# Kernel optimization log

Hardware: AMD Instinct MI355X
Metric: run time of the kernel (lower is better)

## Reference

```python
import jax, jax.numpy as jnp
import numpy as np

NUM_CLASSES = 19
EPS_MEAN = 1e-6   # torch: denominator eps in per-class mean
EPS_COS = 1e-8    # torch CosineSimilarity default eps


def _nearest_resize_labels(target, H, W):
    # torch nn.Upsample(mode='nearest'): in_idx = floor(out_idx * in / out)
    th, tw = target.shape[1], target.shape[2]
    ih = (jnp.arange(H) * th) // H
    iw = (jnp.arange(W) * tw) // W
    return target[:, ih][:, :, iw]  # [B,H,W]


def _class_centers(feat, lab):
    # feat: [B,C,H,W]; lab: [B,H,W] int. Single-pass segment mean by class,
    # then scatter means back to pixels whose label is in [0, NUM_CLASSES).
    B, C, H, W = feat.shape
    f = feat.reshape(B, C, H * W)                 # [B,C,N]
    l = lab.reshape(B, H * W)                      # [B,N]
    onehot = jax.nn.one_hot(l, NUM_CLASSES, dtype=feat.dtype)  # [B,N,K]; out-of-range -> all-zero row
    sums = jnp.einsum('bcn,bnk->bck', f, onehot)   # per-class channel sums
    counts = onehot.sum(axis=1)                    # [B,K]
    means = sums / (counts[:, None, :] + EPS_MEAN) # [B,C,K]
    gathered = jnp.einsum('bck,bnk->bcn', means, onehot)  # mean at each valid pixel, 0 elsewhere
    valid = (l >= 0) & (l < NUM_CLASSES)           # [B,N]
    center = jnp.where(valid[:, None, :], gathered, f)
    return center.reshape(B, C, H, W)


def _cosine_dim1(a, b):
    # torch CosineSimilarity(dim=1): dot / (max(||a||,eps) * max(||b||,eps))
    num = (a * b).sum(axis=1)
    na = jnp.sqrt((a * a).sum(axis=1))
    nb = jnp.sqrt((b * b).sum(axis=1))
    return num / (jnp.maximum(na, EPS_COS) * jnp.maximum(nb, EPS_COS))


def setup_inputs() -> dict:
    key = jax.random.key(0)
    k1, k2, k3 = jax.random.split(key, 3)
    B, C, H, W = 8, 512, 64, 64
    preds_S = jax.random.normal(k1, (B, C, H, W), dtype=jnp.float32)
    preds_T = jax.random.normal(k2, (B, C, H, W), dtype=jnp.float32)
    target = jax.random.randint(k3, (B, 512, 512), 0, NUM_CLASSES, dtype=jnp.int64)
    return {"preds_S": preds_S, "preds_T": preds_T, "target": target}


def reference(preds_S, preds_T, target):
    H, W = preds_S.shape[2], preds_S.shape[3]
    lab = _nearest_resize_labels(target, H, W)     # [B,H,W]
    center_S = _class_centers(preds_S, lab)
    center_T = _class_centers(preds_T, lab)
    pcsim_S = _cosine_dim1(preds_S, center_S)      # [B,H,W]
    pcsim_T = _cosine_dim1(preds_T, center_T)
    return jnp.mean((pcsim_S - pcsim_T) ** 2)
```

## Files before the change

### kernel.cpp

```cpp
#include <hip/hip_runtime.h>

#define NCLS   19
#define NB     8
#define NC     512
#define NHW    4096
#define EPSM   1e-6f
#define EPSC   1e-8f

#define OFF_LABELS   0u
#define OFF_COUNTS   131072u
#define OFF_SUMS_S0  132096u
#define OFF_SUMS_S1  443392u
#define OFF_SUMS_T0  754688u
#define OFF_SUMS_T1  1065984u
#define OFF_NORM_S   1377280u
#define OFF_NORM_T   1378304u
#define OFF_PART     1379328u

template<int CTRL>
__device__ __forceinline__ float dpp_add(float x) {
    int y = __builtin_amdgcn_update_dpp(0, __float_as_int(x), CTRL, 0xf, 0xf, false);
    return x + __int_as_float(y);
}
__device__ __forceinline__ float wave64_sum(float x) {
    x = dpp_add<0x111>(x);
    x = dpp_add<0x112>(x);
    x = dpp_add<0x114>(x);
    x = dpp_add<0x118>(x);
    x = dpp_add<0x142>(x);
    x = dpp_add<0x143>(x);
    return x;
}

__global__ __launch_bounds__(256) void k_labels(const int* __restrict__ target,
                                                int* __restrict__ labels,
                                                float* __restrict__ counts) {
    __shared__ int hist[NCLS];
    const int blk = blockIdx.x;
    const int b = blk >> 3, seg = blk & 7;
    const int t = threadIdx.x;
    if (t < NCLS) hist[t] = 0;
    __syncthreads();
    const int* tb = target + (size_t)b * 512 * 512;
    #pragma unroll
    for (int i = 0; i < 2; ++i) {
        int n = seg * 512 + t + i * 256;
        int y = n >> 6, x = n & 63;
        int l = tb[(y * 8) * 512 + x * 8];
        labels[b * NHW + n] = l;
        if (l >= 0 && l < NCLS) atomicAdd(&hist[l], 1);
    }
    __syncthreads();
    if (t < NCLS) atomicAdd(&counts[b * NCLS + t], (float)hist[t]);
}

__global__ __launch_bounds__(256, 2) void k_sums(const float* __restrict__ fS,
                                                 const float* __restrict__ fT,
                                                 const int* __restrict__ labels,
                                                 float* __restrict__ psS0,
                                                 float* __restrict__ psS1,
                                                 float* __restrict__ psT0,
                                                 float* __restrict__ psT1) {
    const int t = threadIdx.x;
    const int lane = t & 63;
    const int u = (blockIdx.x << 2) + (t >> 6);
    const int b = u >> 10;
    const int rem = u & 1023;
    const int c0 = (rem >> 2) << 1;
    const int tensor = (rem >> 1) & 1;
    const int half = rem & 1;
    const size_t base = ((size_t)(b * NC) + c0) * NHW;
    const float* f = tensor ? fT : fS;
    const float4* p0 = (const float4*)(f + base);
    const float4* p1 = (const float4*)(f + base + NHW);
    const int4* lab4 = (const int4*)(labels + b * NHW);
    const int poff = half << 9;

    float a0[NCLS], a1[NCLS];
    #pragma unroll
    for (int k = 0; k < NCLS; ++k) { a0[k] = a1[k] = 0.f; }

    #pragma unroll 2
    for (int i = 0; i < 8; ++i) {
        const int idx = poff + lane + (i << 6);
        const float4 v0 = p0[idx];
        const float4 v1 = p1[idx];
        const int4 l4 = lab4[idx];
        #pragma unroll
        for (int k = 0; k < NCLS; ++k) {
            const float m0 = (l4.x == k) ? 1.f : 0.f;
            const float m1 = (l4.y == k) ? 1.f : 0.f;
            const float m2 = (l4.z == k) ? 1.f : 0.f;
            const float m3 = (l4.w == k) ? 1.f : 0.f;
            a0[k] += m0 * v0.x + m1 * v0.y + m2 * v0.z + m3 * v0.w;
            a1[k] += m0 * v1.x + m1 * v1.y + m2 * v1.z + m3 * v1.w;
        }
    }
    #pragma unroll
    for (int k = 0; k < NCLS; ++k) {
        a0[k] = wave64_sum(a0[k]);
        a1[k] = wave64_sum(a1[k]);
    }
    if (lane == 63) {
        float* dst = tensor ? (half ? psT1 : psT0) : (half ? psS1 : psS0);
        #pragma unroll
        for (int k = 0; k < NCLS; ++k) {
            *(float2*)(dst + ((size_t)(b * NCLS + k)) * NC + c0) = make_float2(a0[k], a1[k]);
        }
    }
}

__global__ __launch_bounds__(64) void k_means(float* __restrict__ psS0,
                                              const float* __restrict__ psS1,
                                              float* __restrict__ psT0,
                                              const float* __restrict__ psT1,
                                              const float* __restrict__ counts,
                                              float* __restrict__ normS,
                                              float* __restrict__ normT) {
    const int bk = blockIdx.x;
    const int t = threadIdx.x;
    const float inv = 1.f / (counts[bk] + EPSM);
    const size_t row = (size_t)bk * NC;
    float aS = 0.f, aT = 0.f;
    #pragma unroll
    for (int i = 0; i < NC / 64; ++i) {
        const int c = t + i * 64;
        float mS = (psS0[row + c] + psS1[row + c]) * inv;
        float mT = (psT0[row + c] + psT1[row + c]) * inv;
        psS0[row + c] = mS; aS += mS * mS;
        psT0[row + c] = mT; aT += mT * mT;
    }
    aS = wave64_sum(aS);
    aT = wave64_sum(aT);
    if (t == 63) { normS[bk] = sqrtf(aS); normT[bk] = sqrtf(aT); }
}

#define CCH 64
__global__ __launch_bounds__(128) void k_dots(const float* __restrict__ fS,
                                              const float* __restrict__ fT,
                                              const float* __restrict__ meansS,
                                              const float* __restrict__ meansT,
                                              const int* __restrict__ labels,
                                              float* __restrict__ part) {
    __shared__ float mS[NCLS * 65];
    __shared__ float mT[NCLS * 65];
    const int blk = blockIdx.x;
    const int chunk = blk & 7;
    const int tile  = (blk >> 3) & 15;
    const int b     = blk >> 7;
    const int t = threadIdx.x;
    const int c0 = chunk * CCH;
    const int n0 = tile * 256 + t * 2;

    for (int i = t; i < NCLS * CCH; i += 128) {
        const int k = i >> 6, j = i & 63;
        mS[k * 65 + j] = meansS[((size_t)(b * NCLS + k)) * NC + c0 + j];
        mT[k * 65 + j] = meansT[((size_t)(b * NCLS + k)) * NC + c0 + j];
    }
    __syncthreads();

    const int2 l2 = *(const int2*)(labels + b * NHW + n0);
    const int lca = (l2.x >= 0 && l2.x < NCLS) ? l2.x : 0;
    const int lcb = (l2.y >= 0 && l2.y < NCLS) ? l2.y : 0;
    const float* pS = fS + ((size_t)(b * NC + c0)) * NHW + n0;
    const float* pT = fT + ((size_t)(b * NC + c0)) * NHW + n0;
    float dSa = 0.f, dSb = 0.f, nSa = 0.f, nSb = 0.f;
    float dTa = 0.f, dTb = 0.f, nTa = 0.f, nTb = 0.f;
    #pragma unroll 16
    for (int ci = 0; ci < CCH; ++ci) {
        const float2 vS = *(const float2*)(pS + (size_t)ci * NHW);
        const float2 vT = *(const float2*)(pT + (size_t)ci * NHW);
        const float msa = mS[lca * 65 + ci];
        const float msb = mS[lcb * 65 + ci];
        const float mta = mT[lca * 65 + ci];
        const float mtb = mT[lcb * 65 + ci];
        dSa += vS.x * msa; nSa += vS.x * vS.x;
        dSb += vS.y * msb; nSb += vS.y * vS.y;
        dTa += vT.x * mta; nTa += vT.x * vT.x;
        dTb += vT.y * mtb; nTb += vT.y * vT.y;
    }
    const size_t p0 = (size_t)b * NHW + n0;
    *(float2*)(part + ((size_t)(0 * 8 + chunk)) * (NB * NHW) + p0) = make_float2(dSa, dSb);
    *(float2*)(part + ((size_t)(1 * 8 + chunk)) * (NB * NHW) + p0) = make_float2(nSa, nSb);
    *(float2*)(part + ((size_t)(2 * 8 + chunk)) * (NB * NHW) + p0) = make_float2(dTa, dTb);
    *(float2*)(part + ((size_t)(3 * 8 + chunk)) * (NB * NHW) + p0) = make_float2(nTa, nTb);
}

__global__ __launch_bounds__(256) void k_final(const float* __restrict__ part,
                                               const int* __restrict__ labels,
                                               const float* __restrict__ normS,
                                               const float* __restrict__ normT,
                                               float* __restrict__ out) {
    __shared__ float red[4];
    const int p = blockIdx.x * 256 + threadIdx.x;
    const int b = p >> 12;
    float dS = 0.f, nS = 0.f, dT = 0.f, nT = 0.f;
    #pragma unroll
    for (int ch = 0; ch < 8; ++ch) {
        dS += part[((size_t)(0 * 8 + ch)) * (NB * NHW) + p];
        nS += part[((size_t)(1 * 8 + ch)) * (NB * NHW) + p];
        dT += part[((size_t)(2 * 8 + ch)) * (NB * NHW) + p];
        nT += part[((size_t)(3 * 8 + ch)) * (NB * NHW) + p];
    }
    const int l = labels[p];
    float val = 0.f;
    if (l >= 0 && l < NCLS) {
        float cS = dS / (fmaxf(sqrtf(nS), EPSC) * fmaxf(normS[b * NCLS + l], EPSC));
        float cT = dT / (fmaxf(sqrtf(nT), EPSC) * fmaxf(normT[b * NCLS + l], EPSC));
        float d = cS - cT;
        val = d * d;
    }
    val = wave64_sum(val);
    if ((threadIdx.x & 63) == 63) red[threadIdx.x >> 6] = val;
    __syncthreads();
    if (threadIdx.x == 0)
        atomicAdd(out, (red[0] + red[1] + red[2] + red[3]) * (1.f / (NB * NHW)));
}

extern "C" void kernel_launch(void* const* d_in, const int* in_sizes, int n_in,
                              void* d_out, int out_size, void* d_ws, size_t ws_size,
                              hipStream_t stream) {
    (void)in_sizes; (void)n_in; (void)out_size; (void)ws_size;
    const float* fS     = (const float*)d_in[0];
    const float* fT     = (const float*)d_in[1];
    const int*   target = (const int*)d_in[2];

    char* ws = (char*)d_ws;
    int*   labels = (int*)  (ws + OFF_LABELS);
    float* counts = (float*)(ws + OFF_COUNTS);
    float* psS0   = (float*)(ws + OFF_SUMS_S0);
    float* psS1   = (float*)(ws + OFF_SUMS_S1);
    float* psT0   = (float*)(ws + OFF_SUMS_T0);
    float* psT1   = (float*)(ws + OFF_SUMS_T1);
    float* normS  = (float*)(ws + OFF_NORM_S);
    float* normT  = (float*)(ws + OFF_NORM_T);
    float* part   = (float*)(ws + OFF_PART);

    hipMemsetAsync(d_out, 0, sizeof(float), stream);
    hipMemsetAsync(counts, 0, 1024, stream);

    k_labels<<<NB * 8, 256, 0, stream>>>(target, labels, counts);
    k_sums  <<<NB * NC / 2, 256, 0, stream>>>(fS, fT, labels, psS0, psS1, psT0, psT1);
    k_means <<<NB * NCLS, 64, 0, stream>>>(psS0, psS1, psT0, psT1, counts, normS, normT);
    k_dots  <<<NB * 16 * 8, 128, 0, stream>>>(fS, fT, psS0, psT0, labels, part);
    k_final <<<NB * NHW / 256, 256, 0, stream>>>(part, labels, normS, normT,
                                                 (float*)d_out);
}
```

Measured before the change: 223.3 us.

## Replace one-hot masked class sums with LDS atomic scatter-add per wave

```diff
diff --git a/kernel.cpp b/kernel.cpp
--- a/kernel.cpp
+++ b/kernel.cpp
@@ -9,13 +9,11 @@
 
 #define OFF_LABELS   0u
 #define OFF_COUNTS   131072u
-#define OFF_SUMS_S0  132096u
-#define OFF_SUMS_S1  443392u
-#define OFF_SUMS_T0  754688u
-#define OFF_SUMS_T1  1065984u
-#define OFF_NORM_S   1377280u
-#define OFF_NORM_T   1378304u
-#define OFF_PART     1379328u
+#define OFF_SUMS_S   132096u
+#define OFF_SUMS_T   443392u
+#define OFF_NORM_S   754688u
+#define OFF_NORM_T   755712u
+#define OFF_PART     756736u
 
 template<int CTRL>
 __device__ __forceinline__ float dpp_add(float x) {
@@ -34,86 +32,81 @@
 
 __global__ __launch_bounds__(256) void k_labels(const int* __restrict__ target,
                                                 int* __restrict__ labels,
-                                                float* __restrict__ counts) {
+                                                float* __restrict__ counts,
+                                                float* __restrict__ out) {
     __shared__ int hist[NCLS];
-    const int blk = blockIdx.x;
-    const int b = blk >> 3, seg = blk & 7;
-    const int t = threadIdx.x;
+    const int b = blockIdx.x;
+    const int t = threadIdx.x;
+    if (b == 0 && t == 0) out[0] = 0.f;
     if (t < NCLS) hist[t] = 0;
     __syncthreads();
     const int* tb = target + (size_t)b * 512 * 512;
     #pragma unroll
-    for (int i = 0; i < 2; ++i) {
-        int n = seg * 512 + t + i * 256;
+    for (int i = 0; i < 16; ++i) {
+        int n = t + i * 256;
         int y = n >> 6, x = n & 63;
         int l = tb[(y * 8) * 512 + x * 8];
         labels[b * NHW + n] = l;
         if (l >= 0 && l < NCLS) atomicAdd(&hist[l], 1);
     }
     __syncthreads();
-    if (t < NCLS) atomicAdd(&counts[b * NCLS + t], (float)hist[t]);
-}
-
-__global__ __launch_bounds__(256, 2) void k_sums(const float* __restrict__ fS,
-                                                 const float* __restrict__ fT,
-                                                 const int* __restrict__ labels,
-                                                 float* __restrict__ psS0,
-                                                 float* __restrict__ psS1,
-                                                 float* __restrict__ psT0,
-                                                 float* __restrict__ psT1) {
+    if (t < NCLS) counts[b * NCLS + t] = (float)hist[t];
+}
+
+#define RSTRIDE 136
+#define WSTRIDE (2 * RSTRIDE)
+__global__ __launch_bounds__(256) void k_sums(const float* __restrict__ fS,
+                                              const float* __restrict__ fT,
+                                              const int* __restrict__ labels,
+                                              float* __restrict__ sumsS,
+                                              float* __restrict__ sumsT) {
+    __shared__ float acc[4 * WSTRIDE];
     const int t = threadIdx.x;
     const int lane = t & 63;
-    const int u = (blockIdx.x << 2) + (t >> 6);
-    const int b = u >> 10;
-    const int rem = u & 1023;
-    const int c0 = (rem >> 2) << 1;
-    const int tensor = (rem >> 1) & 1;
-    const int half = rem & 1;
-    const size_t base = ((size_t)(b * NC) + c0) * NHW;
-    const float* f = tensor ? fT : fS;
-    const float4* p0 = (const float4*)(f + base);
-    const float4* p1 = (const float4*)(f + base + NHW);
+    const int w = t >> 6;
+    for (int i = t; i < 4 * WSTRIDE; i += 256) acc[i] = 0.f;
+    __syncthreads();
+
+    const int u = (blockIdx.x << 2) + w;
+    const int b = u >> 9;
+    const int c = u & 511;
+    const float4* pS = (const float4*)(fS + (size_t)u * NHW);
+    const float4* pT = (const float4*)(fT + (size_t)u * NHW);
     const int4* lab4 = (const int4*)(labels + b * NHW);
-    const int poff = half << 9;
-
-    float a0[NCLS], a1[NCLS];
-    #pragma unroll
-    for (int k = 0; k < NCLS; ++k) { a0[k] = a1[k] = 0.f; }
-
-    #pragma unroll 2
-    for (int i = 0; i < 8; ++i) {
-        const int idx = poff + lane + (i << 6);
-        const float4 v0 = p0[idx];
-        const float4 v1 = p1[idx];
+
+    float* aS = acc + w * WSTRIDE + (lane >> 4) * 33;
+    float* aT = aS + RSTRIDE;
+
+    #pragma unroll 4
+    for (int i = 0; i < 16; ++i) {
+        const int idx = lane + (i << 6);
+        const float4 vS = pS[idx];
+        const float4 vT = pT[idx];
         const int4 l4 = lab4[idx];
-        #pragma unroll
-        for (int k = 0; k < NCLS; ++k) {
-            const float m0 = (l4.x == k) ? 1.f : 0.f;
-            const float m1 = (l4.y == k) ? 1.f : 0.f;
-            const float m2 = (l4.z == k) ? 1.f : 0.f;
-            const float m3 = (l4.w == k) ? 1.f : 0.f;
-            a0[k] += m0 * v0.x + m1 * v0.y + m2 * v0.z + m3 * v0.w;
-            a1[k] += m0 * v1.x + m1 * v1.y + m2 * v1.z + m3 * v1.w;
-        }
-    }
-    #pragma unroll
-    for (int k = 0; k < NCLS; ++k) {
-        a0[k] = wave64_sum(a0[k]);
-        a1[k] = wave64_sum(a1[k]);
-    }
-    if (lane == 63) {
-        float* dst = tensor ? (half ? psT1 : psT0) : (half ? psS1 : psS0);
-        #pragma unroll
-        for (int k = 0; k < NCLS; ++k) {
-            *(float2*)(dst + ((size_t)(b * NCLS + k)) * NC + c0) = make_float2(a0[k], a1[k]);
-        }
-    }
-}
-
-__global__ __launch_bounds__(64) void k_means(float* __restrict__ psS0,
-                                              const float* __restrict__ psS1,
-                                              float* __restrict__ psT0,
-                                              const float* __restrict__ psT1,
+        const unsigned lx = min((unsigned)l4.x, 19u);
+        const unsigned ly = min((unsigned)l4.y, 19u);
+        const unsigned lz = min((unsigned)l4.z, 19u);
+        const unsigned lw = min((unsigned)l4.w, 19u);
+        atomicAdd(&aS[lx], vS.x); atomicAdd(&aS[ly], vS.y);
+        atomicAdd(&aS[lz], vS.z); atomicAdd(&aS[lw], vS.w);
+        atomicAdd(&aT[lx], vT.x); atomicAdd(&aT[ly], vT.y);
+        atomicAdd(&aT[lz], vT.z); atomicAdd(&aT[lw], vT.w);
+    }
+    __syncthreads();
+    const float* base = acc + w * WSTRIDE;
+    if (lane < NCLS) {
+        float s = base[lane] + base[33 + lane] + base[66 + lane] + base[99 + lane];
+        sumsS[((size_t)(b * NCLS + lane)) * NC + c] = s;
+    } else if (lane >= 32 && lane < 32 + NCLS) {
+        const int l = lane - 32;
+        const float* bT = base + RSTRIDE;
+        float s = bT[l] + bT[33 + l] + bT[66 + l] + bT[99 + l];
+        sumsT[((size_t)(b * NCLS + l)) * NC + c] = s;
+    }
+}
+
+__global__ __launch_bounds__(64) void k_means(float* __restrict__ sumsS,
+                                              float* __restrict__ sumsT,
                                               const float* __restrict__ counts,
                                               float* __restrict__ normS,
                                               float* __restrict__ normT) {
@@ -125,10 +118,8 @@
     #pragma unroll
     for (int i = 0; i < NC / 64; ++i) {
         const int c = t + i * 64;
-        float mS = (psS0[row + c] + psS1[row + c]) * inv;
-        float mT = (psT0[row + c] + psT1[row + c]) * inv;
-        psS0[row + c] = mS; aS += mS * mS;
-        psT0[row + c] = mT; aT += mT * mT;
+        float mS = sumsS[row + c] * inv; sumsS[row + c] = mS; aS += mS * mS;
+        float mT = sumsT[row + c] * inv; sumsT[row + c] = mT; aT += mT * mT;
     }
     aS = wave64_sum(aS);
     aT = wave64_sum(aT);
@@ -228,21 +219,16 @@
     char* ws = (char*)d_ws;
     int*   labels = (int*)  (ws + OFF_LABELS);
     float* counts = (float*)(ws + OFF_COUNTS);
-    float* psS0   = (float*)(ws + OFF_SUMS_S0);
-    float* psS1   = (float*)(ws + OFF_SUMS_S1);
-    float* psT0   = (float*)(ws + OFF_SUMS_T0);
-    float* psT1   = (float*)(ws + OFF_SUMS_T1);
+    float* sumsS  = (float*)(ws + OFF_SUMS_S);
+    float* sumsT  = (float*)(ws + OFF_SUMS_T);
     float* normS  = (float*)(ws + OFF_NORM_S);
     float* normT  = (float*)(ws + OFF_NORM_T);
     float* part   = (float*)(ws + OFF_PART);
 
-    hipMemsetAsync(d_out, 0, sizeof(float), stream);
-    hipMemsetAsync(counts, 0, 1024, stream);
-
-    k_labels<<<NB * 8, 256, 0, stream>>>(target, labels, counts);
-    k_sums  <<<NB * NC / 2, 256, 0, stream>>>(fS, fT, labels, psS0, psS1, psT0, psT1);
-    k_means <<<NB * NCLS, 64, 0, stream>>>(psS0, psS1, psT0, psT1, counts, normS, normT);
-    k_dots  <<<NB * 16 * 8, 128, 0, stream>>>(fS, fT, psS0, psT0, labels, part);
+    k_labels<<<NB, 256, 0, stream>>>(target, labels, counts, (float*)d_out);
+    k_sums  <<<NB * NC / 4, 256, 0, stream>>>(fS, fT, labels, sumsS, sumsT);
+    k_means <<<NB * NCLS, 64, 0, stream>>>(sumsS, sumsT, counts, normS, normT);
+    k_dots  <<<NB * 16 * 8, 128, 0, stream>>>(fS, fT, sumsS, sumsT, labels, part);
     k_final <<<NB * NHW / 256, 256, 0, stream>>>(part, labels, normS, normT,
                                                  (float*)d_out);
 }
```

Result: slower. 335.4 us (+50.2%).
